# Kernel tuning notes

Measured on AMD Instinct MI355X. Metric: run time of the kernel, lower is better.

Reference implementation:

```python
import jax, jax.numpy as jnp
import numpy as np

N, E, F_IN, C, H, L, G, OUT = 10000, 120000, 64, 128, 4, 5, 500, 1801
HL = (L * C) // 2  # JK bidirectional LSTM hidden per direction = 320


def setup_inputs():
    key = jax.random.key(0)
    ks = jax.random.split(key, 20)
    s = 0.05
    p = {}
    p["x"] = jax.random.normal(ks[0], (N, F_IN), jnp.float32)
    p["edge_index"] = jax.random.randint(ks[1], (2, E), 0, N)
    p["batch"] = jnp.sort(jax.random.randint(ks[2], (N,), 0, G))
    p["emb_W"] = jax.random.normal(ks[3], (F_IN, C)) * s
    p["emb_b"] = jnp.zeros((C,))
    p["Wl"] = jax.random.normal(ks[4], (L, C, H * C)) * s
    p["bl"] = jnp.zeros((L, H * C))
    p["Wr"] = jax.random.normal(ks[5], (L, C, H * C)) * s
    p["br"] = jnp.zeros((L, H * C))
    p["att_a"] = jax.random.normal(ks[6], (L, H, C)) * s
    p["conv_b"] = jnp.zeros((L, C))
    p["ln_w"] = jnp.ones((L, C))
    p["ln_b"] = jnp.zeros((L, C))
    p["Wih_f"] = jax.random.normal(ks[7], (4 * HL, C)) * s
    p["Whh_f"] = jax.random.normal(ks[8], (4 * HL, HL)) * s
    p["bih_f"] = jnp.zeros((4 * HL,))
    p["bhh_f"] = jnp.zeros((4 * HL,))
    p["Wih_b"] = jax.random.normal(ks[9], (4 * HL, C)) * s
    p["Whh_b"] = jax.random.normal(ks[10], (4 * HL, HL)) * s
    p["bih_b"] = jnp.zeros((4 * HL,))
    p["bhh_b"] = jnp.zeros((4 * HL,))
    p["jk_w"] = jax.random.normal(ks[11], (2 * HL,)) * s
    p["jk_b"] = jnp.zeros(())
    p["m1_w"] = jax.random.normal(ks[12], (C, C)) * s
    p["m1_b"] = jnp.zeros((C,))
    p["m2_w"] = jax.random.normal(ks[13], (C, OUT)) * s
    p["m2_b"] = jnp.zeros((OUT,))
    p["res_w"] = jax.random.normal(ks[14], (C, OUT)) * s
    p["res_b"] = jnp.zeros((OUT,))
    return p


def _layernorm(x, w, b):
    mu = x.mean(-1, keepdims=True)
    var = ((x - mu) ** 2).mean(-1, keepdims=True)
    return (x - mu) * jax.lax.rsqrt(var + 1e-5) * w + b


def _gatv2(x, src, dst, Wl, bl, Wr, br, a, bias):
    # GATv2Conv, concat=False: mean over heads; eval mode (no dropout)
    xl = (x @ Wl + bl).reshape(N, H, C)   # source projection
    xr = (x @ Wr + br).reshape(N, H, C)   # target projection
    xj = xl[src]                          # [E,H,C] messages from source
    e = jax.nn.leaky_relu(xj + xr[dst], 0.2)
    score = jnp.einsum('ehc,hc->eh', e, a)              # [E,H]
    m = jax.ops.segment_max(score, dst, num_segments=N)  # per-target max
    m = jnp.where(jnp.isfinite(m), m, 0.0)
    ex = jnp.exp(score - m[dst])
    denom = jax.ops.segment_sum(ex, dst, num_segments=N)
    alpha = ex / (denom[dst] + 1e-16)                   # PyG segment softmax
    out = jax.ops.segment_sum(xj * alpha[:, :, None], dst, num_segments=N)
    return out.mean(axis=1) + bias


def _lstm(seq, Wih, Whh, bih, bhh):
    # seq: [L, N, C]; torch gate order i,f,g,o
    def step(carry, xt):
        h, c = carry
        g = xt @ Wih.T + bih + h @ Whh.T + bhh
        i, f, gg, o = jnp.split(g, 4, axis=-1)
        c = jax.nn.sigmoid(f) * c + jax.nn.sigmoid(i) * jnp.tanh(gg)
        h = jax.nn.sigmoid(o) * jnp.tanh(c)
        return (h, c), h
    h0 = jnp.zeros((seq.shape[1], HL), seq.dtype)
    _, hs = jax.lax.scan(step, (h0, h0), seq)
    return hs


def reference(x, edge_index, batch, emb_W, emb_b, Wl, bl, Wr, br, att_a, conv_b, ln_w, ln_b, Wih_f, Whh_f, bih_f, bhh_f, Wih_b, Whh_b, bih_b, bhh_b, jk_w, jk_b, m1_w, m1_b, m2_w, m2_b, res_w, res_b):
    src, dst = edge_index[0], edge_index[1]
    h = x @ emb_W + emb_b
    xs = []
    for l in range(L):
        h = _gatv2(h, src, dst, Wl[l], bl[l], Wr[l], br[l], att_a[l], conv_b[l])
        h = _layernorm(h, ln_w[l], ln_b[l])
        xs.append(h)
    seq = jnp.stack(xs, axis=0)                           # [L,N,C]
    hf = _lstm(seq, Wih_f, Whh_f, bih_f, bhh_f)
    hb = _lstm(seq[::-1], Wih_b, Whh_b, bih_b, bhh_b)[::-1]
    feat = jnp.concatenate([hf, hb], axis=-1)             # [L,N,2*HL]
    scores = feat @ jk_w + jk_b                           # [L,N]
    alpha = jax.nn.softmax(scores, axis=0)
    node = (seq * alpha[:, :, None]).sum(axis=0)          # [N,C]
    cnt = jax.ops.segment_sum(jnp.ones((N,), node.dtype), batch, num_segments=G)
    pooled = jax.ops.segment_sum(node, batch, num_segments=G) / jnp.maximum(cnt, 1.0)[:, None]
    hdn = jax.nn.relu(pooled @ m1_w + m1_b)               # MLPBlock (eval: no dropout)
    return hdn @ m2_w + m2_b + pooled @ res_w + res_b
```

## Files before the change

kernel.cpp:

```cpp
#include <hip/hip_runtime.h>
#include <hip/hip_bf16.h>
#include <math.h>

constexpr int cN   = 10000;
constexpr int cE   = 120000;
constexpr int cFin = 64;
constexpr int cC   = 128;
constexpr int cH   = 4;
constexpr int cL   = 5;
constexpr int cG   = 500;
constexpr int cOUT = 1801;
constexpr int cHL  = 320;
constexpr int c4HL = 4 * cHL;
constexpr int cP   = 2 * c4HL;

typedef short bf16x8 __attribute__((ext_vector_type(8)));
typedef float f32x4 __attribute__((ext_vector_type(4)));

__device__ inline unsigned short f2b(float x) {
    union { __hip_bfloat16 h; unsigned short u; } cv;
    cv.h = __float2bfloat16(x);
    return cv.u;
}
__device__ inline float b2f(unsigned short u) {
    union { unsigned int i; float f; } cv;
    cv.i = ((unsigned int)u) << 16;
    return cv.f;
}
__device__ inline float fsig(float x)  { return 1.f / (1.f + __expf(-x)); }
__device__ inline float ftanh(float x) { return 1.f - 2.f / (__expf(2.f * x) + 1.f); }

#define GLD16(g, l) __builtin_amdgcn_global_load_lds( \
    (const __attribute__((address_space(1))) unsigned int*)(g), \
    (__attribute__((address_space(3))) unsigned int*)(l), 16, 0, 0)

__global__ void fill_i32_kernel(int* __restrict__ p, long n, int v) {
    long i = (long)blockIdx.x * blockDim.x + threadIdx.x;
    if (i < n) p[i] = v;
}
__global__ void copy_i32_kernel(const int* __restrict__ a, int* __restrict__ b, long n) {
    long i = (long)blockIdx.x * blockDim.x + threadIdx.x;
    if (i < n) b[i] = a[i];
}
__global__ void conv_bf16_kernel(const float* __restrict__ a, unsigned short* __restrict__ b, long n) {
    long i = (long)blockIdx.x * blockDim.x + threadIdx.x;
    if (i < n) b[i] = f2b(a[i]);
}
__global__ void init_tail_kernel(float* __restrict__ jks, float* __restrict__ pooled,
                                 float* __restrict__ cnt) {
    long i = (long)blockIdx.x * blockDim.x + threadIdx.x;
    if (i < (long)cL * cN) jks[i] = 0.f;
    else if (i < (long)cL * cN + cG * cC) pooled[i - (long)cL * cN] = 0.f;
    else if (i < (long)cL * cN + cG * cC + cG) cnt[i - (long)cL * cN - cG * cC] = 0.f;
}
__global__ void wproj_prep_kernel(const float* __restrict__ Wl, const float* __restrict__ Wr,
                                  unsigned short* __restrict__ WT) {
    long i = (long)blockIdx.x * blockDim.x + threadIdx.x;
    if (i >= (long)cL * 1024 * 128) return;
    int k = i & 127;
    int n = (int)((i >> 7) & 1023);
    int l = (int)(i >> 17);
    const float* W = (n < 512) ? Wl : Wr;
    int nn = n & 511;
    WT[i] = f2b(W[(size_t)l * 65536 + (size_t)k * 512 + nn]);
}
__global__ void bias_prep_kernel(const float* __restrict__ bl, const float* __restrict__ br,
                                 float* __restrict__ bb) {
    int i = blockIdx.x * blockDim.x + threadIdx.x;
    if (i >= cL * 1024) return;
    int n = i & 1023, l = i >> 10;
    bb[i] = (n < 512) ? bl[l * 512 + n] : br[l * 512 + (n - 512)];
}
__global__ void embw_prep_kernel(const float* __restrict__ W, unsigned short* __restrict__ WT) {
    int i = blockIdx.x * blockDim.x + threadIdx.x;
    if (i >= cC * cFin) return;
    int k = i & 63, n = i >> 6;
    WT[i] = f2b(W[(size_t)k * cC + n]);
}
__global__ void lstm_prep_kernel(const float* __restrict__ Wih, const float* __restrict__ Whh,
                                 const float* __restrict__ bih, const float* __restrict__ bhh,
                                 unsigned short* __restrict__ WihP, unsigned short* __restrict__ WhhP,
                                 float* __restrict__ biasP) {
    long i = (long)blockIdx.x * blockDim.x + threadIdx.x;
    if (i >= (long)c4HL * 449) return;
    int p = (int)(i / 449), c = (int)(i % 449);
    int u = (p >> 6) * 16 + (p & 15);
    int g = (p >> 4) & 3;
    int r = g * cHL + u;
    if (c < cC)       WihP[(size_t)p * cC + c] = f2b(Wih[(size_t)r * cC + c]);
    else if (c < 448) WhhP[(size_t)p * cHL + (c - cC)] = f2b(Whh[(size_t)r * cHL + (c - cC)]);
    else              biasP[p] = bih[r] + bhh[r];
}

__global__ void hist_kernel(const int* __restrict__ dst, int* __restrict__ count) {
    int i = blockIdx.x * blockDim.x + threadIdx.x;
    if (i < cE) atomicAdd(&count[dst[i]], 1);
}
__global__ void scan_kernel(const int* __restrict__ count, int* __restrict__ offs) {
    __shared__ int part[256];
    const int tid = threadIdx.x;
    const int CH = (cN + 255) / 256;
    int base = tid * CH;
    int s = 0;
    for (int i = 0; i < CH; i++) {
        int idx = base + i;
        if (idx < cN) s += count[idx];
    }
    part[tid] = s;
    __syncthreads();
    for (int d = 1; d < 256; d <<= 1) {
        int v = 0;
        if (tid >= d) v = part[tid - d];
        __syncthreads();
        if (tid >= d) part[tid] += v;
        __syncthreads();
    }
    int prefix = (tid == 0) ? 0 : part[tid - 1];
    for (int i = 0; i < CH; i++) {
        int idx = base + i;
        if (idx < cN) { offs[idx] = prefix; prefix += count[idx]; }
    }
    if (tid == 255) offs[cN] = prefix;
}
__global__ void scatter_kernel(const int* __restrict__ src, const int* __restrict__ dst,
                               int* __restrict__ cursor, int* __restrict__ src_csr) {
    int i = blockIdx.x * blockDim.x + threadIdx.x;
    if (i < cE) {
        int pos = atomicAdd(&cursor[dst[i]], 1);
        src_csr[pos] = src[i];
    }
}

template<int HASBIAS, int OUTB, int SWZ>
__global__ __launch_bounds__(256)
void gemm_mfma_kernel(const unsigned short* __restrict__ A1, const unsigned short* __restrict__ B1, int k1,
                      const unsigned short* __restrict__ A2, const unsigned short* __restrict__ B2, int k2,
                      const float* __restrict__ bias, void* __restrict__ Cout, int M, int N, int nbn) {
    int bm, bn;
    if (SWZ) {
        int bid = blockIdx.x;
        int xcd = bid & 7, j = bid >> 3;
        int g   = (j / nbn) * 8 + xcd;
        bm = g << 7;
        bn = (j % nbn) << 7;
        if (bm >= M) return;
    } else {
        bm = blockIdx.y << 7;
        bn = blockIdx.x << 7;
    }
    __shared__ unsigned short lds[2][2][128 * 32];
    const int tid  = threadIdx.x;
    const int lane = tid & 63;
    const int wave = tid >> 6;
    const int wr = (wave >> 1) << 6;
    const int wc = (wave & 1) << 6;
    const int ns1 = k1 >> 5, ns2 = k2 >> 5, ns = ns1 + ns2;

    const int lrow = lane >> 2;
    const int lke  = (lane & 3) << 3;

    auto stage = [&](int s, int buf) {
        const unsigned short *Ab, *Bb;
        int stride, koff;
        if (s < ns1) { Ab = A1; Bb = B1; stride = k1; koff = s << 5; }
        else         { Ab = A2; Bb = B2; stride = k2; koff = (s - ns1) << 5; }
#pragma unroll
        for (int r = 0; r < 2; r++) {
            int ch  = wave * 2 + r;
            int row = ch * 16 + lrow;
            int ga  = bm + row; if (ga >= M) ga = M - 1;
            GLD16(Ab + (size_t)ga * stride + koff + lke, &lds[buf][0][ch * 512]);
            GLD16(Bb + (size_t)(bn + row) * stride + koff + lke, &lds[buf][1][ch * 512]);
        }
    };

    f32x4 acc[4][4];
#pragma unroll
    for (int i = 0; i < 4; i++)
#pragma unroll
        for (int j = 0; j < 4; j++) acc[i][j] = (f32x4){0.f, 0.f, 0.f, 0.f};

    stage(0, 0);
    const int ko  = (lane >> 4) << 3;
    const int rla = lane & 15;
    for (int s = 0; s < ns; s++) {
        int buf = s & 1;
        __syncthreads();
        if (s + 1 < ns) stage(s + 1, buf ^ 1);
        bf16x8 af[4], bff[4];
#pragma unroll
        for (int f = 0; f < 4; f++) {
            af[f]  = *(const bf16x8*)&lds[buf][0][(wr + f * 16 + rla) * 32 + ko];
            bff[f] = *(const bf16x8*)&lds[buf][1][(wc + f * 16 + rla) * 32 + ko];
        }
#pragma unroll
        for (int i = 0; i < 4; i++)
#pragma unroll
            for (int j = 0; j < 4; j++)
                acc[i][j] = __builtin_amdgcn_mfma_f32_16x16x32_bf16(af[i], bff[j], acc[i][j], 0, 0, 0);
    }

#pragma unroll
    for (int i = 0; i < 4; i++) {
#pragma unroll
        for (int v = 0; v < 4; v++) {
            int m = bm + wr + i * 16 + ((lane >> 4) << 2) + v;
            if (m < M) {
#pragma unroll
                for (int j = 0; j < 4; j++) {
                    int n = bn + wc + j * 16 + rla;
                    float val = acc[i][j][v];
                    if (HASBIAS) val += bias[n];
                    if (OUTB) ((unsigned short*)Cout)[(size_t)m * N + n] = f2b(val);
                    else      ((float*)Cout)[(size_t)m * N + n] = val;
                }
            }
        }
    }
}

template<int FIRST, int USEP>
__global__ __launch_bounds__(512)
void gemm_lstm_dual_kernel(const unsigned short* __restrict__ A1f, const unsigned short* __restrict__ A1b,
                           const unsigned short* __restrict__ Bihf, const unsigned short* __restrict__ Bihb,
                           const unsigned short* __restrict__ A2f, const unsigned short* __restrict__ A2b,
                           const unsigned short* __restrict__ Bhhf, const unsigned short* __restrict__ Bhhb,
                           const float* __restrict__ biasPf, const float* __restrict__ biasPb,
                           float* __restrict__ cff, float* __restrict__ cbb,
                           unsigned short* __restrict__ hOutf, unsigned short* __restrict__ hOutb,
                           const float* __restrict__ jkw,
                           float* __restrict__ scoref, float* __restrict__ scoreb,
                           const unsigned short* __restrict__ PfP, const unsigned short* __restrict__ PbP) {
    constexpr int M = cN;
    constexpr int k1 = USEP ? 0 : cC;
    constexpr int k2 = FIRST ? 0 : cHL;
    const int bid = blockIdx.x;
    const int xcd = bid & 7, jj = bid >> 3;
    const int g     = (jj / 10) * 8 + xcd;
    const int inner = jj % 10;
    const int bm = g << 7;
    if (bm >= M) return;
    const int bn = (inner % 5) << 8;
    const int z  = inner / 5;

    const unsigned short* A1 = z ? A1b : A1f;
    const unsigned short* B1 = z ? Bihb : Bihf;
    const unsigned short* A2 = z ? A2b : A2f;
    const unsigned short* B2 = z ? Bhhb : Bhhf;
    const float* biasP = z ? biasPb : biasPf;
    float* cbuf = z ? cbb : cff;
    unsigned short* hOut = z ? hOutb : hOutf;
    const float* jkwz = jkw + (z ? cHL : 0);
    float* score_t = z ? scoreb : scoref;
    const unsigned short* Pst = z ? PbP : PfP;
    const int pcb = (z ? c4HL : 0) + bn;

    __shared__ unsigned short ldsA[2][128 * 32];
    __shared__ unsigned short ldsB[2][256 * 32];
    const int tid  = threadIdx.x;
    const int lane = tid & 63;
    const int wave = tid >> 6;
    const int wr = (wave >> 2) << 6;
    const int wc = (wave & 3) << 6;
    const int ns1 = k1 >> 5, ns2 = k2 >> 5, ns = ns1 + ns2;

    const int lrow = lane >> 2;
    const int lke  = (lane & 3) << 3;

    auto stage = [&](int s, int buf) {
        const unsigned short *Ab, *Bb;
        int stride, koff;
        if (s < ns1) { Ab = A1; Bb = B1; stride = k1; koff = s << 5; }
        else         { Ab = A2; Bb = B2; stride = k2; koff = (s - ns1) << 5; }
        {
            int row = wave * 16 + lrow;
            int ga  = bm + row; if (ga >= M) ga = M - 1;
            GLD16(Ab + (size_t)ga * stride + koff + lke, &ldsA[buf][wave * 512]);
        }
#pragma unroll
        for (int r = 0; r < 2; r++) {
            int ch  = wave * 2 + r;
            int row = ch * 16 + lrow;
            GLD16(Bb + (size_t)(bn + row) * stride + koff + lke, &ldsB[buf][ch * 512]);
        }
    };

    f32x4 acc[4][4];
#pragma unroll
    for (int i = 0; i < 4; i++)
#pragma unroll
        for (int j = 0; j < 4; j++) acc[i][j] = (f32x4){0.f, 0.f, 0.f, 0.f};

    if (ns > 0) stage(0, 0);
    const int ko  = (lane >> 4) << 3;
    const int rla = lane & 15;
    for (int s = 0; s < ns; s++) {
        int buf = s & 1;
        __syncthreads();
        if (s + 1 < ns) stage(s + 1, buf ^ 1);
        bf16x8 af[4], bff[4];
#pragma unroll
        for (int f = 0; f < 4; f++) {
            af[f]  = *(const bf16x8*)&ldsA[buf][(wr + f * 16 + rla) * 32 + ko];
            bff[f] = *(const bf16x8*)&ldsB[buf][(wc + f * 16 + rla) * 32 + ko];
        }
#pragma unroll
        for (int i = 0; i < 4; i++)
#pragma unroll
            for (int j = 0; j < 4; j++)
                acc[i][j] = __builtin_amdgcn_mfma_f32_16x16x32_bf16(af[i], bff[j], acc[i][j], 0, 0, 0);
    }

    float bias4[4];
#pragma unroll
    for (int j = 0; j < 4; j++) bias4[j] = biasP[bn + wc + j * 16 + rla];
    const int u = ((bn + wc) >> 6) * 16 + rla;
    const float jw = jkwz[u];

#pragma unroll
    for (int i = 0; i < 4; i++) {
#pragma unroll
        for (int v = 0; v < 4; v++) {
            int m = bm + wr + i * 16 + ((lane >> 4) << 2) + v;
            bool ok = (m < M);
            float p4[4] = {0.f, 0.f, 0.f, 0.f};
            if (USEP) {
                int mp = ok ? m : M - 1;
#pragma unroll
                for (int j = 0; j < 4; j++)
                    p4[j] = b2f(Pst[(size_t)mp * cP + pcb + wc + j * 16 + rla]);
            }
            float gi = acc[i][0][v] + p4[0] + bias4[0];
            float gf = acc[i][1][v] + p4[1] + bias4[1];
            float gg = acc[i][2][v] + p4[2] + bias4[2];
            float go = acc[i][3][v] + p4[3] + bias4[3];
            float si = fsig(gi);
            float sf = fsig(gf);
            float so = fsig(go);
            float tg = ftanh(gg);
            size_t idx = (size_t)m * cHL + u;
            float cold = (FIRST || !ok) ? 0.f : cbuf[idx];
            float cc = sf * cold + si * tg;
            float hh = so * ftanh(cc);
            if (ok) { cbuf[idx] = cc; hOut[idx] = f2b(hh); }
            float part = ok ? hh * jw : 0.f;
#pragma unroll
            for (int o = 1; o < 16; o <<= 1) part += __shfl_xor(part, o);
            if (rla == 0 && ok) atomicAdd(&score_t[m], part);
        }
    }
}

__global__ __launch_bounds__(256)
void gat_fused_kernel(const unsigned short* __restrict__ xlr, const int* __restrict__ src_csr,
                      const int* __restrict__ offs, const float* __restrict__ att,
                      const float* __restrict__ conv_b, const float* __restrict__ lnw,
                      const float* __restrict__ lnb, float* __restrict__ seq_l,
                      unsigned short* __restrict__ seqb_l) {
    const int wv   = (blockIdx.x * blockDim.x + threadIdx.x) >> 6;
    const int lane = threadIdx.x & 63;
    if (wv >= cN) return;
    const int h   = lane >> 4;
    const int cb  = (lane & 15) << 3;

    bf16x8 xrv = *(const bf16x8*)&xlr[(size_t)wv * 1024 + 512 + lane * 8];
    float xr[8], av[8];
#pragma unroll
    for (int k = 0; k < 8; k++) {
        xr[k] = b2f((unsigned short)xrv[k]);
        av[k] = att[h * 128 + cb + k];
    }

    float m = -INFINITY, l = 0.f;
    float acc[8];
#pragma unroll
    for (int k = 0; k < 8; k++) acc[k] = 0.f;

    const int beg = offs[wv], end = offs[wv + 1];
    int j = beg;
    for (; j + 3 < end; j += 4) {
        int s0 = src_csr[j], s1 = src_csr[j + 1], s2 = src_csr[j + 2], s3 = src_csr[j + 3];
        bf16x8 xv0 = *(const bf16x8*)&xlr[(size_t)s0 * 1024 + lane * 8];
        bf16x8 xv1 = *(const bf16x8*)&xlr[(size_t)s1 * 1024 + lane * 8];
        bf16x8 xv2 = *(const bf16x8*)&xlr[(size_t)s2 * 1024 + lane * 8];
        bf16x8 xv3 = *(const bf16x8*)&xlr[(size_t)s3 * 1024 + lane * 8];
        float x0[8], x1[8], x2[8], x3[8];
        float sc0 = 0.f, sc1 = 0.f, sc2 = 0.f, sc3 = 0.f;
#pragma unroll
        for (int k = 0; k < 8; k++) {
            x0[k] = b2f((unsigned short)xv0[k]);
            x1[k] = b2f((unsigned short)xv1[k]);
            x2[k] = b2f((unsigned short)xv2[k]);
            x3[k] = b2f((unsigned short)xv3[k]);
            float v0 = x0[k] + xr[k]; v0 = v0 > 0.f ? v0 : 0.2f * v0;
            float v1 = x1[k] + xr[k]; v1 = v1 > 0.f ? v1 : 0.2f * v1;
            float v2 = x2[k] + xr[k]; v2 = v2 > 0.f ? v2 : 0.2f * v2;
            float v3 = x3[k] + xr[k]; v3 = v3 > 0.f ? v3 : 0.2f * v3;
            sc0 = fmaf(v0, av[k], sc0);
            sc1 = fmaf(v1, av[k], sc1);
            sc2 = fmaf(v2, av[k], sc2);
            sc3 = fmaf(v3, av[k], sc3);
        }
#pragma unroll
        for (int o = 1; o < 16; o <<= 1) {
            sc0 += __shfl_xor(sc0, o);
            sc1 += __shfl_xor(sc1, o);
            sc2 += __shfl_xor(sc2, o);
            sc3 += __shfl_xor(sc3, o);
        }
        float mn = fmaxf(fmaxf(fmaxf(sc0, sc1), fmaxf(sc2, sc3)), m);
        float r  = __expf(m - mn);
        float p0 = __expf(sc0 - mn);
        float p1 = __expf(sc1 - mn);
        float p2 = __expf(sc2 - mn);
        float p3 = __expf(sc3 - mn);
        l = l * r + p0 + p1 + p2 + p3;
#pragma unroll
        for (int k = 0; k < 8; k++)
            acc[k] = fmaf(acc[k], r,
                          fmaf(p0, x0[k], fmaf(p1, x1[k], fmaf(p2, x2[k], p3 * x3[k]))));
        m = mn;
    }
    for (; j < end; j++) {
        int s0 = src_csr[j];
        bf16x8 xv = *(const bf16x8*)&xlr[(size_t)s0 * 1024 + lane * 8];
        float x[8], sc = 0.f;
#pragma unroll
        for (int k = 0; k < 8; k++) {
            x[k] = b2f((unsigned short)xv[k]);
            float v = x[k] + xr[k];
            v = v > 0.f ? v : 0.2f * v;
            sc = fmaf(v, av[k], sc);
        }
#pragma unroll
        for (int o = 1; o < 16; o <<= 1) sc += __shfl_xor(sc, o);
        float mn = fmaxf(m, sc);
        float r  = __expf(m - mn);
        float p  = __expf(sc - mn);
        l = l * r + p;
#pragma unroll
        for (int k = 0; k < 8; k++) acc[k] = fmaf(acc[k], r, p * x[k]);
        m = mn;
    }
    float inv = 1.f / (l + 1e-16f);

#pragma unroll
    for (int k = 0; k < 8; k++) {
        float v = acc[k] * inv;
        v += __shfl_xor(v, 16);
        v += __shfl_xor(v, 32);
        acc[k] = 0.25f * v + conv_b[cb + k];
    }
    float ssum = 0.f;
#pragma unroll
    for (int k = 0; k < 8; k++) ssum += acc[k];
#pragma unroll
    for (int o = 1; o < 16; o <<= 1) ssum += __shfl_xor(ssum, o);
    float mu = ssum * (1.f / 128.f);
    float vs = 0.f;
#pragma unroll
    for (int k = 0; k < 8; k++) { float d = acc[k] - mu; vs = fmaf(d, d, vs); }
#pragma unroll
    for (int o = 1; o < 16; o <<= 1) vs += __shfl_xor(vs, o);
    float rstd = 1.f / sqrtf(vs * (1.f / 128.f) + 1e-5f);

    float outv[8];
#pragma unroll
    for (int k = 0; k < 8; k++)
        outv[k] = (acc[k] - mu) * rstd * lnw[cb + k] + lnb[cb + k];

    if (h == 0) {
        size_t b = (size_t)wv * 128 + cb;
        float4 o0 = make_float4(outv[0], outv[1], outv[2], outv[3]);
        float4 o1 = make_float4(outv[4], outv[5], outv[6], outv[7]);
        *(float4*)&seq_l[b]     = o0;
        *(float4*)&seq_l[b + 4] = o1;
        bf16x8 ob;
#pragma unroll
        for (int k = 0; k < 8; k++) ob[k] = (short)f2b(outv[k]);
        *(bf16x8*)&seqb_l[b] = ob;
    }
}

__global__ void jk_pool_kernel(const float* __restrict__ seq, const float* __restrict__ score,
                               const int* __restrict__ batch, float* __restrict__ pooled) {
    int wid = (blockIdx.x * blockDim.x + threadIdx.x) >> 6;
    int lane = threadIdx.x & 63;
    if (wid >= cN) return;
    float s[cL], mx = -INFINITY;
#pragma unroll
    for (int l = 0; l < cL; l++) { s[l] = score[(size_t)l * cN + wid]; mx = fmaxf(mx, s[l]); }
    float se = 0.f;
#pragma unroll
    for (int l = 0; l < cL; l++) { s[l] = __expf(s[l] - mx); se += s[l]; }
    float inv = 1.f / se;
    int g = batch[wid];
    float acc0 = 0.f, acc1 = 0.f;
#pragma unroll
    for (int l = 0; l < cL; l++) {
        const float* sp = seq + ((size_t)l * cN + wid) * 128;
        float w = s[l] * inv;
        acc0 += w * sp[lane];
        acc1 += w * sp[lane + 64];
    }
    atomicAdd(&pooled[(size_t)g * 128 + lane], acc0);
    atomicAdd(&pooled[(size_t)g * 128 + lane + 64], acc1);
}

__global__ void count_kernel(const int* __restrict__ batch, float* __restrict__ cnt) {
    int i = blockIdx.x * blockDim.x + threadIdx.x;
    if (i < cN) atomicAdd(&cnt[batch[i]], 1.f);
}

__global__ void div_pool_kernel(float* __restrict__ pooled, const float* __restrict__ cnt) {
    int i = blockIdx.x * blockDim.x + threadIdx.x;
    if (i < cG * 128) pooled[i] /= fmaxf(cnt[i >> 7], 1.f);
}

__global__ __launch_bounds__(256)
void head_fused_kernel(const float* __restrict__ pooled,
                       const float* __restrict__ m1_w, const float* __restrict__ m1_b,
                       const float* __restrict__ m2_w, const float* __restrict__ m2_b,
                       const float* __restrict__ res_w, const float* __restrict__ res_b,
                       float* __restrict__ out) {
    __shared__ float pl[4][128];
    __shared__ float hd[4][128];
    const int tid = threadIdx.x;
    const int r0 = blockIdx.y << 2;
    const int c0 = blockIdx.x << 8;
#pragma unroll
    for (int e = tid; e < 512; e += 256) {
        int r = e >> 7, k = e & 127;
        pl[r][k] = pooled[(size_t)(r0 + r) * 128 + k];
    }
    __syncthreads();
#pragma unroll
    for (int e = tid; e < 512; e += 256) {
        int r = e >> 7, n = e & 127;
        float acc = m1_b[n];
#pragma unroll 8
        for (int k = 0; k < 128; k++) acc = fmaf(pl[r][k], m1_w[k * 128 + n], acc);
        hd[r][n] = fmaxf(acc, 0.f);
    }
    __syncthreads();
    int col = c0 + tid;
    if (col >= cOUT) return;
    float b = m2_b[col] + res_b[col];
    float acc[4] = {b, b, b, b};
    for (int k = 0; k < 128; k++) {
        float w2 = m2_w[(size_t)k * cOUT + col];
        float wr = res_w[(size_t)k * cOUT + col];
#pragma unroll
        for (int r = 0; r < 4; r++)
            acc[r] = fmaf(hd[r][k], w2, fmaf(pl[r][k], wr, acc[r]));
    }
#pragma unroll
    for (int r = 0; r < 4; r++)
        out[(size_t)(r0 + r) * cOUT + col] = acc[r];
}

static inline int ceil_div(long a, long b) { return (int)((a + b - 1) / b); }

template<int OUTB>
static void launch_mfma(const unsigned short* A1, const unsigned short* B1, int k1,
                        const unsigned short* A2, const unsigned short* B2, int k2,
                        const float* bias, void* C, int M, int N, hipStream_t s) {
    dim3 g((N + 127) >> 7, (M + 127) >> 7);
    if (bias) gemm_mfma_kernel<1, OUTB, 0><<<g, 256, 0, s>>>(A1, B1, k1, A2, B2, k2, bias, C, M, N, 0);
    else      gemm_mfma_kernel<0, OUTB, 0><<<g, 256, 0, s>>>(A1, B1, k1, A2, B2, k2, bias, C, M, N, 0);
}
template<int HASBIAS, int OUTB>
static void launch_mfma_swz(const unsigned short* A1, const unsigned short* B1, int k1,
                            const float* bias, void* C, int M, int N, hipStream_t s) {
    int nbn = N >> 7;
    int groups = ((((M + 127) >> 7) + 7) / 8) * 8;
    dim3 g(groups * nbn);
    gemm_mfma_kernel<HASBIAS, OUTB, 1><<<g, 256, 0, s>>>(A1, B1, k1, nullptr, nullptr, 0, bias, C, M, N, nbn);
}

static void fillI(int* p, long n, int v, hipStream_t s) {
    fill_i32_kernel<<<ceil_div(n, 256), 256, 0, s>>>(p, n, v);
}
static void convB(const float* a, unsigned short* b, long n, hipStream_t s) {
    conv_bf16_kernel<<<ceil_div(n, 256), 256, 0, s>>>(a, b, n);
}

extern "C" void kernel_launch(void* const* d_in, const int* in_sizes, int n_in,
                              void* d_out, int out_size, void* d_ws, size_t ws_size,
                              hipStream_t stream) {
    const float* x      = (const float*)d_in[0];
    const int*   ei     = (const int*)d_in[1];
    const int*   batch  = (const int*)d_in[2];
    const float* emb_W  = (const float*)d_in[3];
    const float* emb_b  = (const float*)d_in[4];
    const float* Wl     = (const float*)d_in[5];
    const float* bl     = (const float*)d_in[6];
    const float* Wr     = (const float*)d_in[7];
    const float* br     = (const float*)d_in[8];
    const float* att_a  = (const float*)d_in[9];
    const float* conv_b = (const float*)d_in[10];
    const float* ln_w   = (const float*)d_in[11];
    const float* ln_b   = (const float*)d_in[12];
    const float* Wih_f  = (const float*)d_in[13];
    const float* Whh_f  = (const float*)d_in[14];
    const float* bih_f  = (const float*)d_in[15];
    const float* bhh_f  = (const float*)d_in[16];
    const float* Wih_b  = (const float*)d_in[17];
    const float* Whh_b  = (const float*)d_in[18];
    const float* bih_b  = (const float*)d_in[19];
    const float* bhh_b  = (const float*)d_in[20];
    const float* jk_w   = (const float*)d_in[21];
    const float* m1_w   = (const float*)d_in[23];
    const float* m1_b   = (const float*)d_in[24];
    const float* m2_w   = (const float*)d_in[25];
    const float* m2_b   = (const float*)d_in[26];
    const float* res_w  = (const float*)d_in[27];
    const float* res_b  = (const float*)d_in[28];
    float* out = (float*)d_out;

    const int* src = ei;
    const int* dst = ei + cE;

    char* ws = (char*)d_ws;
    size_t off = 0;
    auto alloc = [&](size_t bytes) -> char* {
        size_t o = (off + 255) & ~(size_t)255;
        off = o + bytes;
        return ws + o;
    };
    unsigned short* x16     = (unsigned short*)alloc((size_t)cN * cFin * 2);
    unsigned short* embWT   = (unsigned short*)alloc((size_t)cC * cFin * 2);
    unsigned short* emb_b16 = (unsigned short*)alloc((size_t)cN * cC * 2);
    float*          seq     = (float*)alloc((size_t)cL * cN * cC * 4);
    unsigned short* seqb16  = (unsigned short*)alloc((size_t)cL * cN * cC * 2);
    unsigned short* WT      = (unsigned short*)alloc((size_t)cL * 1024 * 128 * 2);
    float*          bb      = (float*)alloc((size_t)cL * 1024 * 4);
    unsigned short* WihPfb  = (unsigned short*)alloc((size_t)cP * cC * 2);
    unsigned short* WhhPf   = (unsigned short*)alloc((size_t)c4HL * cHL * 2);
    unsigned short* WhhPb   = (unsigned short*)alloc((size_t)c4HL * cHL * 2);
    float*          biasPf  = (float*)alloc((size_t)c4HL * 4);
    float*          biasPb  = (float*)alloc((size_t)c4HL * 4);
    unsigned short* hf0     = (unsigned short*)alloc((size_t)cN * cHL * 2);
    unsigned short* hf1     = (unsigned short*)alloc((size_t)cN * cHL * 2);
    unsigned short* hbk0    = (unsigned short*)alloc((size_t)cN * cHL * 2);
    unsigned short* hbk1    = (unsigned short*)alloc((size_t)cN * cHL * 2);
    float*          cf      = (float*)alloc((size_t)cN * cHL * 4);
    float*          cbk     = (float*)alloc((size_t)cN * cHL * 4);
    float*          jks     = (float*)alloc((size_t)cL * cN * 4);
    float*          pooled  = (float*)alloc((size_t)cG * cC * 4);
    float*          cnt     = (float*)alloc((size_t)cG * 4);
    int*            offs    = (int*)alloc((size_t)(cN + 1) * 4);
    int*            cursor  = (int*)alloc((size_t)cN * 4);
    int*            src_csr = (int*)alloc((size_t)cE * 4);
    unsigned short* xlr     = (unsigned short*)alloc((size_t)cN * 1024 * 2);
    unsigned short* Pall    = (unsigned short*)alloc((size_t)cL * cN * cP * 2);
    const bool useP = (off <= ws_size);

    unsigned short* WihPf = WihPfb;
    unsigned short* WihPb = WihPfb + (size_t)c4HL * cC;

    hipStream_t s = stream;

    fillI(cursor, cN, 0, s);
    hist_kernel<<<ceil_div(cE, 256), 256, 0, s>>>(dst, cursor);
    scan_kernel<<<1, 256, 0, s>>>(cursor, offs);
    copy_i32_kernel<<<ceil_div(cN, 256), 256, 0, s>>>(offs, cursor, cN);
    scatter_kernel<<<ceil_div(cE, 256), 256, 0, s>>>(src, dst, cursor, src_csr);

    wproj_prep_kernel<<<ceil_div((long)cL * 1024 * 128, 256), 256, 0, s>>>(Wl, Wr, WT);
    bias_prep_kernel<<<ceil_div((long)cL * 1024, 256), 256, 0, s>>>(bl, br, bb);
    embw_prep_kernel<<<ceil_div((long)cC * cFin, 256), 256, 0, s>>>(emb_W, embWT);
    convB(x, x16, (long)cN * cFin, s);
    lstm_prep_kernel<<<ceil_div((long)c4HL * 449, 256), 256, 0, s>>>(
        Wih_f, Whh_f, bih_f, bhh_f, WihPf, WhhPf, biasPf);
    lstm_prep_kernel<<<ceil_div((long)c4HL * 449, 256), 256, 0, s>>>(
        Wih_b, Whh_b, bih_b, bhh_b, WihPb, WhhPb, biasPb);
    init_tail_kernel<<<ceil_div((long)cL * cN + cG * cC + cG, 256), 256, 0, s>>>(jks, pooled, cnt);

    launch_mfma<1>(x16, embWT, cFin, nullptr, nullptr, 0, emb_b, emb_b16, cN, cC, s);

    for (int l = 0; l < cL; l++) {
        const unsigned short* hin = (l == 0) ? emb_b16 : seqb16 + (size_t)(l - 1) * cN * cC;
        launch_mfma_swz<1, 1>(hin, WT + (size_t)l * 1024 * 128, cC,
                              bb + (size_t)l * 1024, xlr, cN, 1024, s);
        gat_fused_kernel<<<ceil_div((long)cN * 64, 256), 256, 0, s>>>(
            xlr, src_csr, offs, att_a + (size_t)l * cH * cC,
            conv_b + (size_t)l * cC, ln_w + (size_t)l * cC, ln_b + (size_t)l * cC,
            seq + (size_t)l * cN * cC, seqb16 + (size_t)l * cN * cC);
    }

    if (useP) {
        launch_mfma_swz<0, 1>(seqb16, WihPfb, cC, nullptr, Pall, cL * cN, cP, s);
    }
    unsigned short* hfb[2]  = {hf0, hf1};
    unsigned short* hbb[2]  = {hbk0, hbk1};
    dim3 lg(80 * 10);
    for (int k = 0; k < cL; k++) {
        int cur = k & 1, prev = cur ^ 1;
        int t = cL - 1 - k;
        const unsigned short* A1f = seqb16 + (size_t)k * cN * cC;
        const unsigned short* A1b = seqb16 + (size_t)t * cN * cC;
        const unsigned short* PfP = Pall + (size_t)k * cN * cP;
        const unsigned short* PbP = Pall + (size_t)t * cN * cP;
        if (useP) {
            if (k == 0)
                gemm_lstm_dual_kernel<1, 1><<<lg, 512, 0, s>>>(
                    nullptr, nullptr, nullptr, nullptr, nullptr, nullptr, nullptr, nullptr,
                    biasPf, biasPb, cf, cbk, hfb[cur], hbb[cur], jk_w,
                    jks + (size_t)k * cN, jks + (size_t)t * cN, PfP, PbP);
            else
                gemm_lstm_dual_kernel<0, 1><<<lg, 512, 0, s>>>(
                    nullptr, nullptr, nullptr, nullptr, hfb[prev], hbb[prev], WhhPf, WhhPb,
                    biasPf, biasPb, cf, cbk, hfb[cur], hbb[cur], jk_w,
                    jks + (size_t)k * cN, jks + (size_t)t * cN, PfP, PbP);
        } else {
            if (k == 0)
                gemm_lstm_dual_kernel<1, 0><<<lg, 512, 0, s>>>(
                    A1f, A1b, WihPf, WihPb, nullptr, nullptr, nullptr, nullptr,
                    biasPf, biasPb, cf, cbk, hfb[cur], hbb[cur], jk_w,
                    jks + (size_t)k * cN, jks + (size_t)t * cN, nullptr, nullptr);
            else
                gemm_lstm_dual_kernel<0, 0><<<lg, 512, 0, s>>>(
                    A1f, A1b, WihPf, WihPb, hfb[prev], hbb[prev], WhhPf, WhhPb,
                    biasPf, biasPb, cf, cbk, hfb[cur], hbb[cur], jk_w,
                    jks + (size_t)k * cN, jks + (size_t)t * cN, nullptr, nullptr);
        }
    }

    jk_pool_kernel<<<ceil_div((long)cN * 64, 256), 256, 0, s>>>(seq, jks, batch, pooled);
    count_kernel<<<ceil_div(cN, 256), 256, 0, s>>>(batch, cnt);
    div_pool_kernel<<<ceil_div((long)cG * 128, 256), 256, 0, s>>>(pooled, cnt);
    head_fused_kernel<<<dim3(ceil_div(cOUT, 256), cG / 4), 256, 0, s>>>(
        pooled, m1_w, m1_b, m2_w, m2_b, res_w, res_b, out);
}
```

Baseline: 683.5 us.

## Split GAT edge aggregation across two waves per node, drop fp32 seq buffer

Each destination node's incoming edges are now split between two wavefronts, whose partial online-softmax states (max, sum, accumulator) are merged through shared memory before the layernorm. This doubles the parallelism available to hide gather latency and shortens each wave's serial edge loop. The fp32 copy of the layer outputs is also removed, and the JK pooling kernel now reads the bf16 copy, which cuts write and read traffic at some precision cost in the pooling step. The merge adds a block-wide barrier, and half the waves sit idle during the epilogue.

```diff
diff --git a/kernel.cpp b/kernel.cpp
--- a/kernel.cpp
+++ b/kernel.cpp
@@ -355,13 +355,18 @@
 void gat_fused_kernel(const unsigned short* __restrict__ xlr, const int* __restrict__ src_csr,
                       const int* __restrict__ offs, const float* __restrict__ att,
                       const float* __restrict__ conv_b, const float* __restrict__ lnw,
-                      const float* __restrict__ lnb, float* __restrict__ seq_l,
-                      unsigned short* __restrict__ seqb_l) {
-    const int wv   = (blockIdx.x * blockDim.x + threadIdx.x) >> 6;
-    const int lane = threadIdx.x & 63;
-    if (wv >= cN) return;
-    const int h   = lane >> 4;
-    const int cb  = (lane & 15) << 3;
+                      const float* __restrict__ lnb, unsigned short* __restrict__ seqb_l) {
+    __shared__ float smacc[2][512];
+    __shared__ float smm[2][4];
+    __shared__ float sml[2][4];
+    const int tid  = threadIdx.x;
+    const int wave = tid >> 6;
+    const int lane = tid & 63;
+    const int nl   = wave >> 1;
+    const int half = wave & 1;
+    const int wv   = blockIdx.x * 2 + nl;
+    const int h    = lane >> 4;
+    const int cb   = (lane & 15) << 3;
 
     bf16x8 xrv = *(const bf16x8*)&xlr[(size_t)wv * 1024 + 512 + lane * 8];
     float xr[8], av[8];
@@ -376,8 +381,11 @@
 #pragma unroll
     for (int k = 0; k < 8; k++) acc[k] = 0.f;
 
-    const int beg = offs[wv], end = offs[wv + 1];
-    int j = beg;
+    const int beg0 = offs[wv], end0 = offs[wv + 1];
+    const int midc = (end0 - beg0 + 1) >> 1;
+    int j   = half ? beg0 + midc : beg0;
+    const int end = half ? end0 : beg0 + midc;
+
     for (; j + 3 < end; j += 4) {
         int s0 = src_csr[j], s1 = src_csr[j + 1], s2 = src_csr[j + 2], s3 = src_csr[j + 3];
         bf16x8 xv0 = *(const bf16x8*)&xlr[(size_t)s0 * 1024 + lane * 8];
@@ -442,8 +450,24 @@
         for (int k = 0; k < 8; k++) acc[k] = fmaf(acc[k], r, p * x[k]);
         m = mn;
     }
+
+    if (half) {
+#pragma unroll
+        for (int k = 0; k < 8; k++) smacc[nl][lane * 8 + k] = acc[k];
+        if ((lane & 15) == 0) { smm[nl][h] = m; sml[nl][h] = l; }
+    }
+    __syncthreads();
+    if (half) return;
+    float m1 = smm[nl][h], l1 = sml[nl][h];
+    float M  = fmaxf(m, m1);
+    float w0 = (m  > -INFINITY) ? __expf(m  - M) : 0.f;
+    float w1 = (m1 > -INFINITY) ? __expf(m1 - M) : 0.f;
+    l = l * w0 + l1 * w1;
+#pragma unroll
+    for (int k = 0; k < 8; k++)
+        acc[k] = acc[k] * w0 + smacc[nl][lane * 8 + k] * w1;
+
     float inv = 1.f / (l + 1e-16f);
-
 #pragma unroll
     for (int k = 0; k < 8; k++) {
         float v = acc[k] * inv;
@@ -471,10 +495,6 @@
 
     if (h == 0) {
         size_t b = (size_t)wv * 128 + cb;
-        float4 o0 = make_float4(outv[0], outv[1], outv[2], outv[3]);
-        float4 o1 = make_float4(outv[4], outv[5], outv[6], outv[7]);
-        *(float4*)&seq_l[b]     = o0;
-        *(float4*)&seq_l[b + 4] = o1;
         bf16x8 ob;
 #pragma unroll
         for (int k = 0; k < 8; k++) ob[k] = (short)f2b(outv[k]);
@@ -482,7 +502,7 @@
     }
 }
 
-__global__ void jk_pool_kernel(const float* __restrict__ seq, const float* __restrict__ score,
+__global__ void jk_pool_kernel(const unsigned short* __restrict__ seqb, const float* __restrict__ score,
                                const int* __restrict__ batch, float* __restrict__ pooled) {
     int wid = (blockIdx.x * blockDim.x + threadIdx.x) >> 6;
     int lane = threadIdx.x & 63;
@@ -498,10 +518,10 @@
     float acc0 = 0.f, acc1 = 0.f;
 #pragma unroll
     for (int l = 0; l < cL; l++) {
-        const float* sp = seq + ((size_t)l * cN + wid) * 128;
+        const unsigned short* sp = seqb + ((size_t)l * cN + wid) * 128;
         float w = s[l] * inv;
-        acc0 += w * sp[lane];
-        acc1 += w * sp[lane + 64];
+        acc0 += w * b2f(sp[lane]);
+        acc1 += w * b2f(sp[lane + 64]);
     }
     atomicAdd(&pooled[(size_t)g * 128 + lane], acc0);
     atomicAdd(&pooled[(size_t)g * 128 + lane + 64], acc1);
@@ -631,7 +651,6 @@
     unsigned short* x16     = (unsigned short*)alloc((size_t)cN * cFin * 2);
     unsigned short* embWT   = (unsigned short*)alloc((size_t)cC * cFin * 2);
     unsigned short* emb_b16 = (unsigned short*)alloc((size_t)cN * cC * 2);
-    float*          seq     = (float*)alloc((size_t)cL * cN * cC * 4);
     unsigned short* seqb16  = (unsigned short*)alloc((size_t)cL * cN * cC * 2);
     unsigned short* WT      = (unsigned short*)alloc((size_t)cL * 1024 * 128 * 2);
     float*          bb      = (float*)alloc((size_t)cL * 1024 * 4);
@@ -683,10 +702,10 @@
         const unsigned short* hin = (l == 0) ? emb_b16 : seqb16 + (size_t)(l - 1) * cN * cC;
         launch_mfma_swz<1, 1>(hin, WT + (size_t)l * 1024 * 128, cC,
                               bb + (size_t)l * 1024, xlr, cN, 1024, s);
-        gat_fused_kernel<<<ceil_div((long)cN * 64, 256), 256, 0, s>>>(
+        gat_fused_kernel<<<cN / 2, 256, 0, s>>>(
             xlr, src_csr, offs, att_a + (size_t)l * cH * cC,
             conv_b + (size_t)l * cC, ln_w + (size_t)l * cC, ln_b + (size_t)l * cC,
-            seq + (size_t)l * cN * cC, seqb16 + (size_t)l * cN * cC);
+            seqb16 + (size_t)l * cN * cC);
     }
 
     if (useP) {
@@ -727,7 +746,7 @@
         }
     }
 
-    jk_pool_kernel<<<ceil_div((long)cN * 64, 256), 256, 0, s>>>(seq, jks, batch, pooled);
+    jk_pool_kernel<<<ceil_div((long)cN * 64, 256), 256, 0, s>>>(seqb16, jks, batch, pooled);
     count_kernel<<<ceil_div(cN, 256), 256, 0, s>>>(batch, cnt);
     div_pool_kernel<<<ceil_div((long)cG * 128, 256), 256, 0, s>>>(pooled, cnt);
     head_fused_kernel<<<dim3(ceil_div(cOUT, 256), cG / 4), 256, 0, s>>>(
```

After: 703.2 us. 2.9% more time.
